# Optimization experiments

Hardware: AMD Instinct MI355X
Metric: run time of the kernel (lower is better)

Reference implementation:

```python
import jax, jax.numpy as jnp
import numpy as np

N_HEADS = 16
D_MODEL = 1024
D_HEAD = D_MODEL // N_HEADS


def setup_inputs() -> dict:
    key = jax.random.key(0)
    k1, k2, k3, k4, k5 = jax.random.split(key, 5)
    B, S = 4, 2048
    scale = 1.0 / np.sqrt(D_MODEL)
    return {
        "x": jax.random.normal(k1, (B, S, D_MODEL), dtype=jnp.float32),
        "W_in": jax.random.normal(k2, (3 * D_MODEL, D_MODEL), dtype=jnp.float32) * scale,
        "b_in": jax.random.normal(k3, (3 * D_MODEL,), dtype=jnp.float32) * 0.02,
        "W_out": jax.random.normal(k4, (D_MODEL, D_MODEL), dtype=jnp.float32) * scale,
        "b_out": jax.random.normal(k5, (D_MODEL,), dtype=jnp.float32) * 0.02,
        "causal_mask": 1,
    }


def reference(x, W_in, b_in, W_out, b_out, causal_mask):
    b, s, d = x.shape
    # in_proj: torch Linear -> x @ W.T + b, then chunk into q,k,v
    qkv = jnp.einsum("bsd,ed->bse", x, W_in) + b_in
    q, k, v = jnp.split(qkv, 3, axis=-1)
    # [b, s, h, dh] -> [b, h, s, dh]
    q = q.reshape(b, s, N_HEADS, D_HEAD).transpose(0, 2, 1, 3)
    k = k.reshape(b, s, N_HEADS, D_HEAD).transpose(0, 2, 1, 3)
    v = v.reshape(b, s, N_HEADS, D_HEAD).transpose(0, 2, 1, 3)
    # scores [b, h, s, s]
    qk = jnp.einsum("bhqd,bhkd->bhqk", q, k)
    if causal_mask:
        mask = jnp.triu(jnp.ones((s, s), dtype=bool), k=1)
        qk = jnp.where(mask, -jnp.inf, qk)
    qk = qk / jnp.sqrt(jnp.float32(D_HEAD))
    attn = jax.nn.softmax(qk, axis=-1)
    out = jnp.einsum("bhqk,bhkd->bhqd", attn, v)  # [b, h, s, dh]
    out = out.transpose(0, 2, 1, 3).reshape(b, s, d)
    return jnp.einsum("bsd,ed->bse", out, W_out) + b_out
```

## Files before the change

### kernel.cpp

```cpp
#include <hip/hip_runtime.h>
#include <hip/hip_bf16.h>
#include <cstdint>
#include <cstddef>

typedef short bf16x8 __attribute__((ext_vector_type(8)));
typedef float f32x4 __attribute__((ext_vector_type(4)));

#define SEQ 2048
#define NH 16
#define DH 64
#define DM 1024

typedef __attribute__((address_space(1))) const void gvoid_t;
typedef __attribute__((address_space(3))) void lvoid_t;

__device__ __forceinline__ unsigned short f2bf(float f) {
  union { float f; unsigned int u; } v; v.f = f;
  return (unsigned short)((v.u + 0x7FFFu + ((v.u >> 16) & 1u)) >> 16);
}

__device__ __forceinline__ void barx() {
  asm volatile("" ::: "memory");
  __builtin_amdgcn_s_barrier();
  asm volatile("" ::: "memory");
}
#define VMC4()  asm volatile("s_waitcnt vmcnt(4)" ::: "memory")
#define SCHED0() __builtin_amdgcn_sched_barrier(0)

__global__ void __launch_bounds__(256) k_cvt3(const float* __restrict__ x,
                                              const float* __restrict__ wi,
                                              const float* __restrict__ wo,
                                              unsigned short* __restrict__ xb,
                                              unsigned short* __restrict__ wib,
                                              unsigned short* __restrict__ wob) {
  int bidx = blockIdx.x;
  const float* src; unsigned short* dst; int base;
  if (bidx < 8192)       { src = x;  dst = xb;  base = bidx; }
  else if (bidx < 11264) { src = wi; dst = wib; base = bidx - 8192; }
  else                   { src = wo; dst = wob; base = bidx - 11264; }
  int i = (base * 256 + threadIdx.x) * 4;
  float4 v = *(const float4*)(src + i);
  ushort4 o;
  o.x = f2bf(v.x); o.y = f2bf(v.y); o.z = f2bf(v.z); o.w = f2bf(v.w);
  *(ushort4*)(dst + i) = o;
}

#define LDS_T 16384

__device__ __forceinline__ void stage_half(const unsigned short* __restrict__ G,
                                           int row0, int kt, unsigned short* lds,
                                           int Rhalf, int rstat, int cOff, int wave) {
#pragma unroll
  for (int pc = 0; pc < 2; ++pc) {
    const int R = Rhalf + pc * 64;
    __builtin_amdgcn_global_load_lds(
        (gvoid_t*)(G + (size_t)(row0 + R + rstat) * DM + kt * 64 + cOff),
        (lvoid_t*)(lds + (R + wave * 8) * 64), 16, 0, 0);
  }
}

__device__ __forceinline__ void lda8(const unsigned short* lds, int rb, int l16,
                                     int sw0, int sw1, bf16x8 (&a)[8]) {
#pragma unroll
  for (int f = 0; f < 4; ++f) {
    const unsigned short* p = lds + (rb + f * 16 + l16) * 64;
    a[f * 2 + 0] = *(const bf16x8*)(p + sw0);
    a[f * 2 + 1] = *(const bf16x8*)(p + sw1);
  }
}

__device__ __forceinline__ void ldb4(const unsigned short* lds, int rb, int l16,
                                     int sw0, int sw1, bf16x8 (&b)[4]) {
#pragma unroll
  for (int g = 0; g < 2; ++g) {
    const unsigned short* p = lds + (rb + g * 16 + l16) * 64;
    b[g * 2 + 0] = *(const bf16x8*)(p + sw0);
    b[g * 2 + 1] = *(const bf16x8*)(p + sw1);
  }
}

template <int MQ, int NQ>
__device__ __forceinline__ void mfma_quad(const bf16x8 (&a)[8], const bf16x8 (&b)[4],
                                          f32x4 (&acc)[8][4]) {
  __builtin_amdgcn_s_setprio(1);
#pragma unroll
  for (int f = 0; f < 4; ++f)
#pragma unroll
    for (int g = 0; g < 2; ++g) {
      f32x4 c = acc[MQ * 4 + f][NQ * 2 + g];
      c = __builtin_amdgcn_mfma_f32_16x16x32_bf16(a[f * 2 + 0], b[g * 2 + 0], c, 0, 0, 0);
      c = __builtin_amdgcn_mfma_f32_16x16x32_bf16(a[f * 2 + 1], b[g * 2 + 1], c, 0, 0, 0);
      acc[MQ * 4 + f][NQ * 2 + g] = c;
    }
  __builtin_amdgcn_s_setprio(0);
}

__device__ __forceinline__ void gemm256(const unsigned short* __restrict__ A,
                                        const unsigned short* __restrict__ Bt,
                                        unsigned short* lA, unsigned short* lB,
                                        int m0, int n0, f32x4 (&acc)[8][4]) {
  const int t = threadIdx.x;
  const int wave = t >> 6, lane = t & 63, quad = lane >> 4, l16 = lane & 15;
  (void)lane;
  const int rstat = t >> 3;
  const int cOff = ((t & 7) ^ (rstat & 7)) * 8;
  const int sw0 = (quad ^ (l16 & 7)) * 8;
  const int sw1 = ((quad ^ 4) ^ (l16 & 7)) * 8;
  const int wm = wave >> 2, wn = wave & 3;
  const int arb0 = wm * 64, arb1 = 128 + wm * 64;
  const int brb0 = wn * 32, brb1 = 128 + wn * 32;
  const int NT = DM / 64;

  bf16x8 af[8], b0[4], b1[4];

  stage_half(A,  m0, 0, lA, 0,   rstat, cOff, wave);
  stage_half(Bt, n0, 0, lB, 0,   rstat, cOff, wave);
  stage_half(A,  m0, 0, lA, 128, rstat, cOff, wave);
  stage_half(Bt, n0, 0, lB, 128, rstat, cOff, wave);
  stage_half(A,  m0, 1, lA + LDS_T, 0,   rstat, cOff, wave);
  stage_half(Bt, n0, 1, lB + LDS_T, 128, rstat, cOff, wave);
  VMC4();
  barx();

  for (int t0 = 0; t0 < NT; t0 += 2) {
    const int t2 = (t0 + 2 < NT) ? t0 + 2 : NT - 1;
    const int t3 = (t0 + 3 < NT) ? t0 + 3 : NT - 1;
    lda8(lA, arb0, l16, sw0, sw1, af);
    ldb4(lB, brb0, l16, sw0, sw1, b0);
    ldb4(lB, brb1, l16, sw0, sw1, b1);
    stage_half(A, m0, t0 + 1, lA + LDS_T, 128, rstat, cOff, wave);
    barx();
    mfma_quad<0, 0>(af, b0, acc);
    SCHED0(); barx();
    stage_half(Bt, n0, t0 + 1, lB + LDS_T, 0, rstat, cOff, wave);
    barx();
    mfma_quad<0, 1>(af, b1, acc);
    SCHED0();
    lda8(lA, arb1, l16, sw0, sw1, af);
    barx();
    stage_half(A, m0, t2, lA, 0, rstat, cOff, wave);
    barx();
    mfma_quad<1, 1>(af, b1, acc);
    SCHED0(); barx();
    stage_half(Bt, n0, t2, lB, 128, rstat, cOff, wave);
    VMC4();
    barx();
    mfma_quad<1, 0>(af, b0, acc);
    SCHED0(); barx();
    lda8(lA + LDS_T, arb0, l16, sw0, sw1, af);
    ldb4(lB + LDS_T, brb0, l16, sw0, sw1, b0);
    ldb4(lB + LDS_T, brb1, l16, sw0, sw1, b1);
    stage_half(A, m0, t2, lA, 128, rstat, cOff, wave);
    barx();
    mfma_quad<0, 0>(af, b0, acc);
    SCHED0(); barx();
    stage_half(Bt, n0, t2, lB, 0, rstat, cOff, wave);
    barx();
    mfma_quad<0, 1>(af, b1, acc);
    SCHED0();
    lda8(lA + LDS_T, arb1, l16, sw0, sw1, af);
    barx();
    stage_half(A, m0, t3, lA + LDS_T, 0, rstat, cOff, wave);
    barx();
    mfma_quad<1, 1>(af, b1, acc);
    SCHED0(); barx();
    stage_half(Bt, n0, t3, lB + LDS_T, 128, rstat, cOff, wave);
    VMC4();
    barx();
    mfma_quad<1, 0>(af, b0, acc);
    SCHED0(); barx();
  }
}

__global__ void __launch_bounds__(512, 2) k_gemm_qkv(
    const unsigned short* __restrict__ X,
    const unsigned short* __restrict__ Wi,
    const float* __restrict__ bias,
    unsigned short* __restrict__ Qo,
    unsigned short* __restrict__ Ko,
    unsigned short* __restrict__ Vto) {
  __shared__ unsigned short lA[2 * LDS_T];
  __shared__ unsigned short lB[2 * LDS_T];
  const int t = threadIdx.x;
  const int wave = t >> 6, lane = t & 63, quad = lane >> 4, l16 = lane & 15;
  (void)lane;
  const int wm = wave >> 2, wn = wave & 3;
  const int nwg = 32 * 12;
  const int bid = blockIdx.x;
  const int swz = (bid & 7) * (nwg / 8) + (bid >> 3);
  const int m0 = (swz / 12) * 256, n0 = (swz % 12) * 256;

  f32x4 acc[8][4];
  f32x4 zf = {0.f, 0.f, 0.f, 0.f};
#pragma unroll
  for (int i = 0; i < 8; ++i)
#pragma unroll
    for (int j = 0; j < 4; ++j) acc[i][j] = zf;

  gemm256(X, Wi, lA, lB, m0, n0, acc);

  const float SCALE = 0.18033688011112042f;
  const int sel = n0 >> 10;
#pragma unroll
  for (int nf = 0; nf < 4; ++nf) {
    const int gcol = n0 + (nf >> 1) * 128 + wn * 32 + (nf & 1) * 16 + l16;
    const float bv = bias[gcol];
    const int c = gcol & 1023;
    const int hh = c >> 6, dh = c & 63;
    if (sel == 0) {
#pragma unroll
      for (int mf = 0; mf < 8; ++mf) {
        const int grow = m0 + (mf >> 2) * 128 + wm * 64 + (mf & 3) * 16 + quad * 4;
        const int bb = grow >> 11, sb = grow & 2047;
        unsigned short* qp = Qo + ((size_t)(bb * NH + hh) * SEQ + sb) * DH + dh;
#pragma unroll
        for (int r = 0; r < 4; ++r)
          qp[(size_t)r * DH] = f2bf((acc[mf][nf][r] + bv) * SCALE);
      }
    } else if (sel == 1) {
#pragma unroll
      for (int mf = 0; mf < 8; ++mf) {
        const int grow = m0 + (mf >> 2) * 128 + wm * 64 + (mf & 3) * 16 + quad * 4;
        const int bb = grow >> 11, sb = grow & 2047;
        unsigned short* kp = Ko + ((size_t)(bb * NH + hh) * SEQ + sb) * DH + dh;
#pragma unroll
        for (int r = 0; r < 4; ++r)
          kp[(size_t)r * DH] = f2bf(acc[mf][nf][r] + bv);
      }
    } else {
#pragma unroll
      for (int mf = 0; mf < 8; ++mf) {
        const int grow = m0 + (mf >> 2) * 128 + wm * 64 + (mf & 3) * 16 + quad * 4;
        const int bb = grow >> 11, sb = grow & 2047;
        ushort4 pk;
        pk.x = f2bf(acc[mf][nf][0] + bv);
        pk.y = f2bf(acc[mf][nf][1] + bv);
        pk.z = f2bf(acc[mf][nf][2] + bv);
        pk.w = f2bf(acc[mf][nf][3] + bv);
        *(ushort4*)(&Vto[((size_t)(bb * NH + hh) * DH + dh) * SEQ + sb]) = pk;
      }
    }
  }
}

#define ASTR 72

__global__ void __launch_bounds__(256, 4) k_attn(
    const unsigned short* __restrict__ Q,
    const unsigned short* __restrict__ K,
    const unsigned short* __restrict__ Vt,
    unsigned short* __restrict__ Ao,
    const int* __restrict__ causal_p) {
  __shared__ unsigned short lK[64 * 64];
  __shared__ unsigned short lV[64 * 64];
  __shared__ unsigned short lP[2][4][16 * ASTR];

  const int t = threadIdx.x;
  const int wave = t >> 6, lane = t & 63, quad = lane >> 4, l16 = lane & 15;
  const int id = blockIdx.x;
  const int cxcd = id & 7, w = id >> 3;
  const int x = w & 15, g = (w >> 4) * 8 + cxcd;
  const int h = g & 15, b = g >> 4;
  const int qtA = x, qtB = 31 - x;
  const int bh = b * NH + h;
  const int causal = causal_p[0];
  const int ktA = causal ? qtA : 31;
  const int ktB = causal ? qtB : 31;
  const int q0A = qtA * 64, q0B = qtB * 64;

  const unsigned short* Qb = Q + (size_t)bh * SEQ * DH;
  const unsigned short* Kb = K + (size_t)bh * SEQ * DH;
  const unsigned short* Vb = Vt + (size_t)bh * DH * SEQ;

  bf16x8 qA0 = *(const bf16x8*)(&Qb[(q0A + wave * 16 + l16) * DH + quad * 8]);
  bf16x8 qA1 = *(const bf16x8*)(&Qb[(q0A + wave * 16 + l16) * DH + 32 + quad * 8]);
  bf16x8 qB0 = *(const bf16x8*)(&Qb[(q0B + wave * 16 + l16) * DH + quad * 8]);
  bf16x8 qB1 = *(const bf16x8*)(&Qb[(q0B + wave * 16 + l16) * DH + 32 + quad * 8]);

  f32x4 zf = {0.f, 0.f, 0.f, 0.f};
  f32x4 oA[4], oB[4];
  for (int i = 0; i < 4; ++i) { oA[i] = zf; oB[i] = zf; }
  f32x4 lacA = zf, lacB = zf;

  bf16x8 ones;
#pragma unroll
  for (int i = 0; i < 8; ++i) ones[i] = (short)0x3F80;

  unsigned short* lPa = &lP[0][wave][0];
  unsigned short* lPb = &lP[1][wave][0];

  const int i0 = t, i1 = 256 + t;
  const int rr0 = i0 >> 3, cc0 = ((i0 & 7) ^ (rr0 & 7)) * 8;
  const int rr1 = i1 >> 3, cc1 = ((i1 & 7) ^ (rr1 & 7)) * 8;
  const int kof0 = rr0 * DH + cc0, kof1 = rr1 * DH + cc1;
  const int vof0 = rr0 * SEQ + cc0, vof1 = rr1 * SEQ + cc1;
  const int rbase = l16 * 64;
  const int sw0 = ((quad ^ (l16 & 7)) * 8);
  const int sw1 = (((quad ^ 4) ^ (l16 & 7)) * 8);

  for (int kt = 0; kt <= ktB; ++kt) {
    const int k0 = kt * 64;
    const bool doA = (kt <= ktA);

    __syncthreads();
    __builtin_amdgcn_global_load_lds((gvoid_t*)(Kb + (size_t)k0 * DH + kof0),
                                     (lvoid_t*)&lK[wave * 512], 16, 0, 0);
    __builtin_amdgcn_global_load_lds((gvoid_t*)(Kb + (size_t)k0 * DH + kof1),
                                     (lvoid_t*)&lK[wave * 512 + 2048], 16, 0, 0);
    __builtin_amdgcn_global_load_lds((gvoid_t*)(Vb + k0 + vof0),
                                     (lvoid_t*)&lV[wave * 512], 16, 0, 0);
    __builtin_amdgcn_global_load_lds((gvoid_t*)(Vb + k0 + vof1),
                                     (lvoid_t*)&lV[wave * 512 + 2048], 16, 0, 0);
    __syncthreads();

    f32x4 sA[4], sB[4];
#pragma unroll
    for (int nt = 0; nt < 4; ++nt) {
      bf16x8 kf0 = *(const bf16x8*)(&lK[nt * 1024 + rbase + sw0]);
      bf16x8 kf1 = *(const bf16x8*)(&lK[nt * 1024 + rbase + sw1]);
      f32x4 zb = zf;
      zb = __builtin_amdgcn_mfma_f32_16x16x32_bf16(qB0, kf0, zb, 0, 0, 0);
      zb = __builtin_amdgcn_mfma_f32_16x16x32_bf16(qB1, kf1, zb, 0, 0, 0);
      sB[nt] = zb;
      if (doA) {
        f32x4 za = zf;
        za = __builtin_amdgcn_mfma_f32_16x16x32_bf16(qA0, kf0, za, 0, 0, 0);
        za = __builtin_amdgcn_mfma_f32_16x16x32_bf16(qA1, kf1, za, 0, 0, 0);
        sA[nt] = za;
      }
    }

    if (causal && kt == qtB) {
#pragma unroll
      for (int nt = 0; nt < 4; ++nt) {
        int kcol = k0 + nt * 16 + l16;
#pragma unroll
        for (int r = 0; r < 4; ++r)
          if (kcol > q0B + wave * 16 + quad * 4 + r) sB[nt][r] = -1e30f;
      }
    }
    if (causal && doA && kt == qtA) {
#pragma unroll
      for (int nt = 0; nt < 4; ++nt) {
        int kcol = k0 + nt * 16 + l16;
#pragma unroll
        for (int r = 0; r < 4; ++r)
          if (kcol > q0A + wave * 16 + quad * 4 + r) sA[nt][r] = -1e30f;
      }
    }

#pragma unroll
    for (int nt = 0; nt < 4; ++nt)
#pragma unroll
      for (int r = 0; r < 4; ++r)
        lPb[(quad * 4 + r) * ASTR + nt * 16 + l16] =
            f2bf(__builtin_amdgcn_exp2f(sB[nt][r]));
    if (doA) {
#pragma unroll
      for (int nt = 0; nt < 4; ++nt)
#pragma unroll
        for (int r = 0; r < 4; ++r)
          lPa[(quad * 4 + r) * ASTR + nt * 16 + l16] =
              f2bf(__builtin_amdgcn_exp2f(sA[nt][r]));
    }

    asm volatile("s_waitcnt lgkmcnt(0)" ::: "memory");

    bf16x8 pB0 = *(const bf16x8*)(&lPb[l16 * ASTR + quad * 8]);
    bf16x8 pB1 = *(const bf16x8*)(&lPb[l16 * ASTR + 32 + quad * 8]);
    bf16x8 pA0 = pB0, pA1 = pB1;
    if (doA) {
      pA0 = *(const bf16x8*)(&lPa[l16 * ASTR + quad * 8]);
      pA1 = *(const bf16x8*)(&lPa[l16 * ASTR + 32 + quad * 8]);
    }

    lacB = __builtin_amdgcn_mfma_f32_16x16x32_bf16(pB0, ones, lacB, 0, 0, 0);
    lacB = __builtin_amdgcn_mfma_f32_16x16x32_bf16(pB1, ones, lacB, 0, 0, 0);
    if (doA) {
      lacA = __builtin_amdgcn_mfma_f32_16x16x32_bf16(pA0, ones, lacA, 0, 0, 0);
      lacA = __builtin_amdgcn_mfma_f32_16x16x32_bf16(pA1, ones, lacA, 0, 0, 0);
    }

#pragma unroll
    for (int nt = 0; nt < 4; ++nt) {
      bf16x8 vf0 = *(const bf16x8*)(&lV[nt * 1024 + rbase + sw0]);
      bf16x8 vf1 = *(const bf16x8*)(&lV[nt * 1024 + rbase + sw1]);
      oB[nt] = __builtin_amdgcn_mfma_f32_16x16x32_bf16(pB0, vf0, oB[nt], 0, 0, 0);
      oB[nt] = __builtin_amdgcn_mfma_f32_16x16x32_bf16(pB1, vf1, oB[nt], 0, 0, 0);
      if (doA) {
        oA[nt] = __builtin_amdgcn_mfma_f32_16x16x32_bf16(pA0, vf0, oA[nt], 0, 0, 0);
        oA[nt] = __builtin_amdgcn_mfma_f32_16x16x32_bf16(pA1, vf1, oA[nt], 0, 0, 0);
      }
    }
  }

#pragma unroll
  for (int r = 0; r < 4; ++r) {
    float invB = 1.0f / lacB[r];
    float invA = 1.0f / lacA[r];
#pragma unroll
    for (int nt = 0; nt < 4; ++nt) {
      int dh = nt * 16 + l16;
      int qgB = q0B + wave * 16 + quad * 4 + r;
      Ao[(size_t)(b * SEQ + qgB) * DM + h * DH + dh] = f2bf(oB[nt][r] * invB);
      int qgA = q0A + wave * 16 + quad * 4 + r;
      Ao[(size_t)(b * SEQ + qgA) * DM + h * DH + dh] = f2bf(oA[nt][r] * invA);
    }
  }
}

__device__ __forceinline__ void gemm_tile_bt(const unsigned short* __restrict__ A,
                                             const unsigned short* __restrict__ Bt,
                                             unsigned short* lA, unsigned short* lB,
                                             int m0, int n0, f32x4 (&acc)[4][4]) {
  const int t = threadIdx.x;
  const int wave = t >> 6, lane = t & 63, quad = lane >> 4, l16 = lane & 15;
  (void)lane;
  const int mh = (wave >> 1) * 64, nh = (wave & 1) * 64;
  int row_[4], c_[4];
#pragma unroll
  for (int r = 0; r < 4; ++r) {
    int i = r * 256 + t;
    row_[r] = i >> 3;
    c_[r] = ((i & 7) ^ ((i >> 3) & 7)) * 8;
  }
  const int sw0 = ((quad) ^ (l16 & 7)) * 8;
  const int sw1 = ((quad ^ 4) ^ (l16 & 7)) * 8;
  for (int k0 = 0; k0 < DM; k0 += 64) {
    __syncthreads();
#pragma unroll
    for (int r = 0; r < 4; ++r) {
      __builtin_amdgcn_global_load_lds((gvoid_t*)&A[(size_t)(m0 + row_[r]) * DM + k0 + c_[r]],
                                       (lvoid_t*)&lA[(r * 4 + wave) * 512], 16, 0, 0);
      __builtin_amdgcn_global_load_lds((gvoid_t*)&Bt[(size_t)(n0 + row_[r]) * DM + k0 + c_[r]],
                                       (lvoid_t*)&lB[(r * 4 + wave) * 512], 16, 0, 0);
    }
    __syncthreads();
    bf16x8 af[4], bfr[4];
#pragma unroll
    for (int i = 0; i < 4; ++i)
      af[i] = *(const bf16x8*)(&lA[(mh + i * 16 + l16) * 64 + sw0]);
#pragma unroll
    for (int i = 0; i < 4; ++i)
      bfr[i] = *(const bf16x8*)(&lB[(nh + i * 16 + l16) * 64 + sw0]);
#pragma unroll
    for (int mt = 0; mt < 4; ++mt)
#pragma unroll
      for (int nt = 0; nt < 4; ++nt)
        acc[mt][nt] = __builtin_amdgcn_mfma_f32_16x16x32_bf16(af[mt], bfr[nt], acc[mt][nt], 0, 0, 0);
#pragma unroll
    for (int i = 0; i < 4; ++i)
      af[i] = *(const bf16x8*)(&lA[(mh + i * 16 + l16) * 64 + sw1]);
#pragma unroll
    for (int i = 0; i < 4; ++i)
      bfr[i] = *(const bf16x8*)(&lB[(nh + i * 16 + l16) * 64 + sw1]);
#pragma unroll
    for (int mt = 0; mt < 4; ++mt)
#pragma unroll
      for (int nt = 0; nt < 4; ++nt)
        acc[mt][nt] = __builtin_amdgcn_mfma_f32_16x16x32_bf16(af[mt], bfr[nt], acc[mt][nt], 0, 0, 0);
  }
}

__global__ void __launch_bounds__(256, 2) k_gemm_out(
    const unsigned short* __restrict__ Ai,
    const unsigned short* __restrict__ Wo,
    const float* __restrict__ bias,
    float* __restrict__ C) {
  __shared__ unsigned short lA[128 * 64];
  __shared__ unsigned short lB[128 * 64];
  const int t = threadIdx.x;
  const int wave = t >> 6, lane = t & 63, quad = lane >> 4, l16 = lane & 15;
  (void)lane;
  const int m0 = blockIdx.x * 128, n0 = blockIdx.y * 128;
  f32x4 acc[4][4];
  f32x4 zf = {0.f, 0.f, 0.f, 0.f};
  for (int i = 0; i < 4; ++i)
    for (int j = 0; j < 4; ++j) acc[i][j] = zf;
  gemm_tile_bt(Ai, Wo, lA, lB, m0, n0, acc);
  const int mh = (wave >> 1) * 64, nh = (wave & 1) * 64;
#pragma unroll
  for (int nt = 0; nt < 4; ++nt) {
    int gcol = n0 + nh + nt * 16 + l16;
    float bv = bias[gcol];
#pragma unroll
    for (int mt = 0; mt < 4; ++mt) {
      int rowbase = m0 + mh + mt * 16 + quad * 4;
#pragma unroll
      for (int r = 0; r < 4; ++r)
        C[(size_t)(rowbase + r) * DM + gcol] = acc[mt][nt][r] + bv;
    }
  }
}

extern "C" void kernel_launch(void* const* d_in, const int* in_sizes, int n_in,
                              void* d_out, int out_size, void* d_ws, size_t ws_size,
                              hipStream_t stream) {
  (void)in_sizes; (void)n_in; (void)out_size; (void)ws_size;
  const float* x     = (const float*)d_in[0];
  const float* W_in  = (const float*)d_in[1];
  const float* b_in  = (const float*)d_in[2];
  const float* W_out = (const float*)d_in[3];
  const float* b_out = (const float*)d_in[4];
  const int* causal  = (const int*)d_in[5];
  float* out = (float*)d_out;
  char* ws = (char*)d_ws;

  unsigned short* xb  = (unsigned short*)(ws + 0);
  unsigned short* Aob = (unsigned short*)(ws + 0);
  unsigned short* Wib = (unsigned short*)(ws + (size_t)(16 << 20));
  unsigned short* Wob = (unsigned short*)(ws + (size_t)(22 << 20));
  unsigned short* Qb  = (unsigned short*)(ws + (size_t)(24 << 20));
  unsigned short* Kb  = (unsigned short*)(ws + (size_t)(40 << 20));
  unsigned short* Vtb = (unsigned short*)(ws + (size_t)(56 << 20));

  k_cvt3<<<12288, 256, 0, stream>>>(x, W_in, W_out, xb, Wib, Wob);
  k_gemm_qkv<<<384, 512, 0, stream>>>(xb, Wib, b_in, Qb, Kb, Vtb);
  k_attn<<<1024, 256, 0, stream>>>(Qb, Kb, Vtb, Aob, causal);
  k_gemm_out<<<dim3(64, 8), 256, 0, stream>>>(Aob, Wob, b_out, out);
}
```

Before: 248.0 us.

## Deepen GEMM software pipeline with double-buffered register fragments and occupancy 1

Restructures the 256x256 GEMM main loop so LDS fragment loads for the next quadrant are issued one MFMA phase earlier into separate register sets (afX/afY, bAX/bAY). More global stage loads are kept in flight, using vmcnt(6)/vmcnt(8) instead of vmcnt(4). The QKV GEMM launch bound drops to one block per SM so it can use the extra registers. The aim is to hide LDS and global latency behind MFMAs, at the cost of lower occupancy and a trickier barrier and ordering schedule.

```diff
diff --git a/kernel.cpp b/kernel.cpp
--- a/kernel.cpp
+++ b/kernel.cpp
@@ -24,7 +24,8 @@
   __builtin_amdgcn_s_barrier();
   asm volatile("" ::: "memory");
 }
-#define VMC4()  asm volatile("s_waitcnt vmcnt(4)" ::: "memory")
+#define VMC6()  asm volatile("s_waitcnt vmcnt(6)" ::: "memory")
+#define VMC8()  asm volatile("s_waitcnt vmcnt(8)" ::: "memory")
 #define SCHED0() __builtin_amdgcn_sched_barrier(0)
 
 __global__ void __launch_bounds__(256) k_cvt3(const float* __restrict__ x,
@@ -111,68 +112,71 @@
   const int brb0 = wn * 32, brb1 = 128 + wn * 32;
   const int NT = DM / 64;
 
-  bf16x8 af[8], b0[4], b1[4];
+  bf16x8 afX[8], afY[8], bAX[4], bAY[4], bB[4];
 
   stage_half(A,  m0, 0, lA, 0,   rstat, cOff, wave);
   stage_half(Bt, n0, 0, lB, 0,   rstat, cOff, wave);
   stage_half(A,  m0, 0, lA, 128, rstat, cOff, wave);
   stage_half(Bt, n0, 0, lB, 128, rstat, cOff, wave);
   stage_half(A,  m0, 1, lA + LDS_T, 0,   rstat, cOff, wave);
-  stage_half(Bt, n0, 1, lB + LDS_T, 128, rstat, cOff, wave);
-  VMC4();
+  stage_half(Bt, n0, 1, lB + LDS_T, 0,   rstat, cOff, wave);
+  stage_half(A,  m0, 1, lA + LDS_T, 128, rstat, cOff, wave);
+  VMC6();
   barx();
-
-  for (int t0 = 0; t0 < NT; t0 += 2) {
-    const int t2 = (t0 + 2 < NT) ? t0 + 2 : NT - 1;
-    const int t3 = (t0 + 3 < NT) ? t0 + 3 : NT - 1;
-    lda8(lA, arb0, l16, sw0, sw1, af);
-    ldb4(lB, brb0, l16, sw0, sw1, b0);
-    ldb4(lB, brb1, l16, sw0, sw1, b1);
-    stage_half(A, m0, t0 + 1, lA + LDS_T, 128, rstat, cOff, wave);
-    barx();
-    mfma_quad<0, 0>(af, b0, acc);
-    SCHED0(); barx();
-    stage_half(Bt, n0, t0 + 1, lB + LDS_T, 0, rstat, cOff, wave);
-    barx();
-    mfma_quad<0, 1>(af, b1, acc);
-    SCHED0();
-    lda8(lA, arb1, l16, sw0, sw1, af);
-    barx();
+  lda8(lA, arb0, l16, sw0, sw1, afX);
+  ldb4(lB, brb0, l16, sw0, sw1, bAX);
+
+  for (int t0i = 0; t0i < NT; t0i += 2) {
+    const int t2 = (t0i + 2 < NT) ? t0i + 2 : NT - 1;
+    const int t3 = (t0i + 3 < NT) ? t0i + 3 : NT - 1;
+    ldb4(lB, brb1, l16, sw0, sw1, bB);
+    stage_half(Bt, n0, t0i + 1, lB + LDS_T, 128, rstat, cOff, wave);
+    barx();
+    mfma_quad<0, 0>(afX, bAX, acc);
+    SCHED0(); barx();
+    lda8(lA, arb1, l16, sw0, sw1, afY);
     stage_half(A, m0, t2, lA, 0, rstat, cOff, wave);
     barx();
-    mfma_quad<1, 1>(af, b1, acc);
-    SCHED0(); barx();
+    mfma_quad<0, 1>(afX, bB, acc);
+    SCHED0(); barx();
+    stage_half(Bt, n0, t2, lB, 0, rstat, cOff, wave);
+    VMC8();
+    barx();
+    mfma_quad<1, 1>(afY, bB, acc);
+    SCHED0(); barx();
+    lda8(lA + LDS_T, arb0, l16, sw0, sw1, afX);
+    ldb4(lB + LDS_T, brb0, l16, sw0, sw1, bAY);
+    stage_half(A, m0, t2, lA, 128, rstat, cOff, wave);
+    VMC6();
+    barx();
+    mfma_quad<1, 0>(afY, bAX, acc);
+    SCHED0(); barx();
+    ldb4(lB + LDS_T, brb1, l16, sw0, sw1, bB);
     stage_half(Bt, n0, t2, lB, 128, rstat, cOff, wave);
-    VMC4();
-    barx();
-    mfma_quad<1, 0>(af, b0, acc);
-    SCHED0(); barx();
-    lda8(lA + LDS_T, arb0, l16, sw0, sw1, af);
-    ldb4(lB + LDS_T, brb0, l16, sw0, sw1, b0);
-    ldb4(lB + LDS_T, brb1, l16, sw0, sw1, b1);
-    stage_half(A, m0, t2, lA, 128, rstat, cOff, wave);
-    barx();
-    mfma_quad<0, 0>(af, b0, acc);
-    SCHED0(); barx();
-    stage_half(Bt, n0, t2, lB, 0, rstat, cOff, wave);
-    barx();
-    mfma_quad<0, 1>(af, b1, acc);
-    SCHED0();
-    lda8(lA + LDS_T, arb1, l16, sw0, sw1, af);
-    barx();
+    barx();
+    mfma_quad<0, 0>(afX, bAY, acc);
+    SCHED0(); barx();
+    lda8(lA + LDS_T, arb1, l16, sw0, sw1, afY);
     stage_half(A, m0, t3, lA + LDS_T, 0, rstat, cOff, wave);
     barx();
-    mfma_quad<1, 1>(af, b1, acc);
-    SCHED0(); barx();
-    stage_half(Bt, n0, t3, lB + LDS_T, 128, rstat, cOff, wave);
-    VMC4();
-    barx();
-    mfma_quad<1, 0>(af, b0, acc);
-    SCHED0(); barx();
-  }
-}
-
-__global__ void __launch_bounds__(512, 2) k_gemm_qkv(
+    mfma_quad<0, 1>(afX, bB, acc);
+    SCHED0(); barx();
+    stage_half(Bt, n0, t3, lB + LDS_T, 0, rstat, cOff, wave);
+    VMC8();
+    barx();
+    mfma_quad<1, 1>(afY, bB, acc);
+    SCHED0(); barx();
+    lda8(lA, arb0, l16, sw0, sw1, afX);
+    ldb4(lB, brb0, l16, sw0, sw1, bAX);
+    stage_half(A, m0, t3, lA + LDS_T, 128, rstat, cOff, wave);
+    VMC6();
+    barx();
+    mfma_quad<1, 0>(afY, bAY, acc);
+    SCHED0(); barx();
+  }
+}
+
+__global__ void __launch_bounds__(512, 1) k_gemm_qkv(
     const unsigned short* __restrict__ X,
     const unsigned short* __restrict__ Wi,
     const float* __restrict__ bias,
```

Measured after the change: 272.5 us. +9.9%, slower.
